# Kernel tuning notes

Measured on AMD Instinct MI355X. Metric: run time of the kernel, lower is better.

## Reference

```python
import jax, jax.numpy as jnp
import numpy as np

D_MODEL = 512
NHEAD = 8
D_HEAD = D_MODEL // NHEAD
SCALE = D_HEAD ** -0.5
EPS = 1e-8


def setup_inputs() -> dict:
    key = jax.random.key(0)
    ks = jax.random.split(key, 12)
    B, N = 4, 2048
    s = D_MODEL ** -0.5
    return {
        "Q_input": jax.random.normal(ks[0], (B, N, D_MODEL), jnp.float32),
        "KV_input": jax.random.normal(ks[1], (B, N, D_MODEL), jnp.float32),
        "SC": jax.random.uniform(ks[2], (B, N, N), jnp.float32),
        "Wq_w": jax.random.normal(ks[3], (D_MODEL, D_MODEL), jnp.float32) * s,
        "Wq_b": jnp.zeros((D_MODEL,), jnp.float32),
        "Wk_w": jax.random.normal(ks[4], (D_MODEL, D_MODEL), jnp.float32) * s,
        "Wk_b": jnp.zeros((D_MODEL,), jnp.float32),
        "Wv_w": jax.random.normal(ks[5], (D_MODEL, D_MODEL), jnp.float32) * s,
        "Wv_b": jnp.zeros((D_MODEL,), jnp.float32),
        "gate_w": jax.random.normal(ks[6], (), jnp.float32),
        "gate_b": jnp.zeros((), jnp.float32),
        "out_w": jax.random.normal(ks[7], (D_MODEL, D_MODEL), jnp.float32) * s,
        "out_b": jnp.zeros((D_MODEL,), jnp.float32),
    }


def reference(Q_input, KV_input, SC, Wq_w, Wq_b, Wk_w, Wk_b, Wv_w, Wv_b,
              gate_w, gate_b, out_w, out_b):
    B, N, _ = Q_input.shape
    # projections -> [B, H, N, d_head]
    def proj(x, w, b):
        y = x @ w.T + b
        return y.reshape(B, N, NHEAD, D_HEAD).transpose(0, 2, 1, 3)
    Q = proj(Q_input, Wq_w, Wq_b)
    K = proj(KV_input, Wk_w, Wk_b)
    V = proj(KV_input, Wv_w, Wv_b)
    # scores [B, H, N, N]
    scores = jnp.einsum('bhqd,bhkd->bhqk', Q, K) * SCALE
    # per-edge gate: sigmoid(w*SC + b), broadcast over heads
    g = jax.nn.sigmoid(SC * gate_w + gate_b)  # [B, N, N]
    scores = scores + jnp.log(g + EPS)[:, None, :, :]
    attn = jax.nn.softmax(scores, axis=-1)
    out = jnp.einsum('bhqk,bhkd->bhqd', attn, V)
    out = out.transpose(0, 2, 1, 3).reshape(B, N, D_MODEL)
    return out @ out_w.T + out_b
```

## Files before the change

kernel.cpp:

```cpp
#include <hip/hip_runtime.h>

typedef unsigned short u16;
typedef unsigned int u32;
typedef __attribute__((ext_vector_type(4))) float f32x4;
typedef __attribute__((ext_vector_type(8))) short s16x8;
typedef __attribute__((ext_vector_type(4))) u16 u16x4;

#define L2E 1.4426950408889634f
#define QSCALE 0.18033688011112042f

__device__ __forceinline__ float bf2f(u16 u) {
    union { u32 i; float f; } v; v.i = ((u32)u) << 16; return v.f;
}
__device__ __forceinline__ u16 f2bf(float f) {
    union { float f; u32 i; } v; v.f = f;
    return (u16)((v.i + 0x7fffu + ((v.i >> 16) & 1u)) >> 16);
}
__device__ __forceinline__ u16 f2bf_rn(float f) {
    union { float f; u32 i; } v; v.f = f;
    return (u16)((v.i + 0x8000u) >> 16);
}

__device__ __forceinline__ void gl2lds16(const u16* g, u16* l) {
    __builtin_amdgcn_global_load_lds(
        (const __attribute__((address_space(1))) void*)g,
        (__attribute__((address_space(3))) void*)l, 16, 0, 0);
}

__global__ __launch_bounds__(256) void conv_kernel(
    const float* __restrict__ s0, const float* __restrict__ s1,
    const float* __restrict__ s2, const float* __restrict__ s3,
    const float* __restrict__ s4, const float* __restrict__ s5,
    u16* __restrict__ dst)
{
    int e = (blockIdx.x * 256 + threadIdx.x) * 4;
    const float* src; int off;
    if      (e < 4194304) { src = s0; off = e; }
    else if (e < 8388608) { src = s1; off = e - 4194304; }
    else if (e < 8650752) { src = s2; off = e - 8388608; }
    else if (e < 8912896) { src = s3; off = e - 8650752; }
    else if (e < 9175040) { src = s4; off = e - 8912896; }
    else                  { src = s5; off = e - 9175040; }
    f32x4 f = *(const f32x4*)(src + off);
    u16x4 o;
#pragma unroll
    for (int j = 0; j < 4; ++j) o[j] = f2bf(f[j]);
    *(u16x4*)(dst + e) = o;
}

__global__ __launch_bounds__(256) void lg_kernel(
    const float* __restrict__ SC, const float* __restrict__ gwp,
    const float* __restrict__ gbp, u16* __restrict__ LGx)
{
    const int flat = blockIdx.x * 256 + threadIdx.x;
    const int lane = flat & 63;
    const int kt   = (flat >> 6) & 31;
    const int t16  = (flat >> 11) & 127;
    const int b    = flat >> 18;
    const int l16 = lane & 15, quad = lane >> 4;
    const float tA = -gwp[0] * L2E, tB = -gbp[0] * L2E;
    const float* row = SC + ((size_t)b * 2048 + t16 * 16 + l16) * 2048
                          + kt * 64 + quad * 4;
    __align__(16) u16 tmp[16];
#pragma unroll
    for (int kk = 0; kk < 4; ++kk) {
        f32x4 x = *(const f32x4*)(row + kk * 16);
#pragma unroll
        for (int reg = 0; reg < 4; ++reg) {
            float g = __builtin_amdgcn_rcpf(
                1.0f + __builtin_amdgcn_exp2f(tA * x[reg] + tB)) + 1e-8f;
            tmp[kk * 4 + reg] = f2bf(__builtin_amdgcn_logf(g));
        }
    }
    u16* dst = LGx + (size_t)flat * 16;
    *(uint4*)dst       = *(uint4*)tmp;
    *(uint4*)(dst + 8) = *(uint4*)(tmp + 8);
}

__device__ __forceinline__ void gemm_core(
    const u16* __restrict__ A, const u16* __restrict__ Bw,
    int m0, int n0, u16* As, u16* Bs, f32x4 acc[4][4])
{
    const int tid = threadIdx.x;
    const int lane = tid & 63, w = tid >> 6;
    const int wm = w >> 1, wn = w & 1;
    const int l16 = lane & 15, quad = lane >> 4;
    const int srow = (lane >> 2), sch = (lane & 3) * 8;
    const f32x4 vzero = {0.f, 0.f, 0.f, 0.f};
#pragma unroll
    for (int i = 0; i < 4; ++i)
#pragma unroll
        for (int j = 0; j < 4; ++j) acc[i][j] = vzero;

    for (int kt = 0; kt < 16; ++kt) {
#pragma unroll
        for (int j = 0; j < 2; ++j) {
            int row = w * 32 + j * 16 + srow;
            gl2lds16(&A[(size_t)(m0 + row) * 512 + kt * 32 + sch],
                     &As[w * 1024 + j * 512]);
            gl2lds16(&Bw[(size_t)(n0 + row) * 512 + kt * 32 + sch],
                     &Bs[w * 1024 + j * 512]);
        }
        __syncthreads();
        s16x8 af[4], bfr[4];
#pragma unroll
        for (int mt = 0; mt < 4; ++mt)
            af[mt] = *(const s16x8*)&As[(wm * 64 + mt * 16 + l16) * 32 + quad * 8];
#pragma unroll
        for (int nt = 0; nt < 4; ++nt)
            bfr[nt] = *(const s16x8*)&Bs[(wn * 64 + nt * 16 + l16) * 32 + quad * 8];
#pragma unroll
        for (int mt = 0; mt < 4; ++mt)
#pragma unroll
            for (int nt = 0; nt < 4; ++nt)
                acc[mt][nt] = __builtin_amdgcn_mfma_f32_16x16x32_bf16(
                    af[mt], bfr[nt], acc[mt][nt], 0, 0, 0);
        __syncthreads();
    }
}

__global__ __launch_bounds__(256) void proj_kernel(
    const u16* __restrict__ cQin, const u16* __restrict__ cKV,
    const u16* __restrict__ cW,
    const float* __restrict__ bq, const float* __restrict__ bk,
    const float* __restrict__ bv,
    u16* __restrict__ Qh, u16* __restrict__ Kh, u16* __restrict__ Vt)
{
    __shared__ __align__(16) u16 As[128 * 32];
    __shared__ __align__(16) u16 Bs[128 * 32];
    const int job = blockIdx.z;
    const u16* A = (job == 0) ? cQin : cKV;
    const u16* W = cW + (size_t)job * 262144;
    const float* bias = (job == 0) ? bq : (job == 1 ? bk : bv);
    const int m0 = blockIdx.y * 128, n0 = blockIdx.x * 128;
    f32x4 acc[4][4];
    gemm_core(A, W, m0, n0, As, Bs, acc);

    const int tid = threadIdx.x, lane = tid & 63, w = tid >> 6;
    const int wm = w >> 1, wn = w & 1, l16 = lane & 15, quad = lane >> 4;
#pragma unroll
    for (int nt = 0; nt < 4; ++nt) {
        int j = n0 + wn * 64 + nt * 16 + l16;
        float bj = bias[j];
        int h = j >> 6, d = j & 63;
#pragma unroll
        for (int mt = 0; mt < 4; ++mt) {
            int trow = m0 + wm * 64 + mt * 16 + quad * 4;
            int bb = trow >> 11, nn = trow & 2047;
            int bh = bb * 8 + h;
            if (job == 2) {
                u16x4 pv;
#pragma unroll
                for (int reg = 0; reg < 4; ++reg) pv[reg] = f2bf(acc[mt][nt][reg] + bj);
                *(u16x4*)&Vt[(size_t)(bh * 64 + d) * 2048 + nn] = pv;
            } else if (job == 0) {
#pragma unroll
                for (int reg = 0; reg < 4; ++reg)
                    Qh[(size_t)(bh * 2048 + nn + reg) * 64 + d] =
                        f2bf((acc[mt][nt][reg] + bj) * QSCALE);
            } else {
#pragma unroll
                for (int reg = 0; reg < 4; ++reg)
                    Kh[(size_t)(bh * 2048 + nn + reg) * 64 + d] =
                        f2bf(acc[mt][nt][reg] + bj);
            }
        }
    }
}

__global__ __launch_bounds__(512, 4) void attn_kernel(
    const u16* __restrict__ Qh, const u16* __restrict__ Kh,
    const u16* __restrict__ Vt, const u16* __restrict__ LGx,
    u16* __restrict__ Ob)
{
    __shared__ __align__(16) u16 Ks[2][4096];
    __shared__ __align__(16) u16 Vs[2][4096];
    __shared__ __align__(16) u16 Plds[8][16][68];
    const int tid = threadIdx.x;
    const int w = tid >> 6, lane = tid & 63;
    const int l16 = lane & 15, quad = lane >> 4;
    const int b = blockIdx.z, head = blockIdx.y, qg = blockIdx.x;
    const int bh = b * 8 + head;
    const int q0 = qg * 128 + w * 16;
    const int t16 = qg * 8 + w;
    const u16* Qp = Qh + (size_t)bh * 131072;
    const u16* Kp = Kh + (size_t)bh * 131072;
    const u16* Vp = Vt + (size_t)bh * 131072;
    const u16* LGt = LGx + ((size_t)((b * 128 + t16) * 32) * 64 + lane) * 16;
    const f32x4 vzero = {0.f, 0.f, 0.f, 0.f};

    const int sr = lane >> 3;
    const int scw = ((lane & 7) ^ sr) * 8;
    const int slab = (w & 3) * 16;
    const bool isK = (w < 4);
    const u16* sG0 = isK ? (Kp + (size_t)(slab + sr) * 64 + scw)
                         : (Vp + (size_t)(slab + sr) * 2048 + scw);
    const u16* sG1 = isK ? (Kp + (size_t)(slab + 8 + sr) * 64 + scw)
                         : (Vp + (size_t)(slab + 8 + sr) * 2048 + scw);
    const size_t sAdv = isK ? 4096 : 64;
    u16* sL0 = isK ? &Ks[0][slab * 64] : &Vs[0][slab * 64];
    u16* sL1 = isK ? &Ks[0][(slab + 8) * 64] : &Vs[0][(slab + 8) * 64];

    s16x8 qf[2];
#pragma unroll
    for (int kc = 0; kc < 2; ++kc)
        qf[kc] = *(const s16x8*)&Qp[(size_t)(q0 + l16) * 64 + kc * 32 + quad * 8];
    f32x4 o[4];
    float lsum = 0.f;
#pragma unroll
    for (int dn = 0; dn < 4; ++dn) o[dn] = vzero;

    gl2lds16(sG0, sL0);
    gl2lds16(sG1, sL1);

    for (int kt = 0; kt < 32; ++kt) {
        __syncthreads();
        const int cur = kt & 1;
        if (kt < 31) {
            const int nxt = cur ^ 1;
            gl2lds16(sG0 + (size_t)(kt + 1) * sAdv, sL0 + nxt * 4096);
            gl2lds16(sG1 + (size_t)(kt + 1) * sAdv, sL1 + nxt * 4096);
        }
        const u16* Kb = &Ks[cur][0];
        const u16* Vb = &Vs[cur][0];
        __align__(16) u16 lgv[16];
        *(uint4*)lgv       = *(const uint4*)(LGt + (size_t)kt * 1024);
        *(uint4*)(lgv + 8) = *(const uint4*)(LGt + (size_t)kt * 1024 + 8);

        f32x4 st[4];
#pragma unroll
        for (int kc = 0; kc < 2; ++kc) {
            s16x8 kf[4];
#pragma unroll
            for (int kk = 0; kk < 4; ++kk)
                kf[kk] = *(const s16x8*)&Kb[(kk * 16 + l16) * 64 +
                                            ((kc * 4 + quad) ^ (l16 & 7)) * 8];
#pragma unroll
            for (int kk = 0; kk < 4; ++kk)
                st[kk] = __builtin_amdgcn_mfma_f32_16x16x32_bf16(
                    kf[kk], qf[kc], kc == 0 ? vzero : st[kk], 0, 0, 0);
        }
#pragma unroll
        for (int kk = 0; kk < 4; ++kk) {
            u16x4 pp;
#pragma unroll
            for (int reg = 0; reg < 4; ++reg) {
                float p = __builtin_amdgcn_exp2f(st[kk][reg] +
                                                 bf2f(lgv[kk * 4 + reg]));
                lsum += p;
                pp[reg] = f2bf_rn(p);
            }
            *(u16x4*)&Plds[w][l16][kk * 16 + quad * 4] = pp;
        }
#pragma unroll
        for (int kc = 0; kc < 2; ++kc) {
            s16x8 pf = *(const s16x8*)&Plds[w][l16][kc * 32 + quad * 8];
            s16x8 vf[4];
#pragma unroll
            for (int dn = 0; dn < 4; ++dn)
                vf[dn] = *(const s16x8*)&Vb[(dn * 16 + l16) * 64 +
                                            ((kc * 4 + quad) ^ (l16 & 7)) * 8];
#pragma unroll
            for (int dn = 0; dn < 4; ++dn)
                o[dn] = __builtin_amdgcn_mfma_f32_16x16x32_bf16(
                    pf, vf[dn], o[dn], 0, 0, 0);
        }
    }
    lsum += __shfl_xor(lsum, 16, 64);
    lsum += __shfl_xor(lsum, 32, 64);
    float inv = __builtin_amdgcn_rcpf(lsum);
#pragma unroll
    for (int reg = 0; reg < 4; ++reg) {
        float invr = __shfl(inv, quad * 4 + reg, 64);
        int trow = b * 2048 + q0 + quad * 4 + reg;
#pragma unroll
        for (int dn = 0; dn < 4; ++dn)
            Ob[(size_t)trow * 512 + head * 64 + dn * 16 + l16] =
                f2bf(o[dn][reg] * invr);
    }
}

__global__ __launch_bounds__(256) void out_kernel(
    const u16* __restrict__ Ob, const u16* __restrict__ cWo,
    const float* __restrict__ bo, float* __restrict__ out)
{
    __shared__ __align__(16) u16 As[128 * 32];
    __shared__ __align__(16) u16 Bs[128 * 32];
    const int m0 = blockIdx.y * 128, n0 = blockIdx.x * 128;
    f32x4 acc[4][4];
    gemm_core(Ob, cWo, m0, n0, As, Bs, acc);
    const int tid = threadIdx.x, lane = tid & 63, w = tid >> 6;
    const int wm = w >> 1, wn = w & 1, l16 = lane & 15, quad = lane >> 4;
#pragma unroll
    for (int nt = 0; nt < 4; ++nt) {
        int j = n0 + wn * 64 + nt * 16 + l16;
        float bj = bo[j];
#pragma unroll
        for (int mt = 0; mt < 4; ++mt) {
            int t = m0 + wm * 64 + mt * 16 + quad * 4;
#pragma unroll
            for (int reg = 0; reg < 4; ++reg)
                out[(size_t)(t + reg) * 512 + j] = acc[mt][nt][reg] + bj;
        }
    }
}

extern "C" void kernel_launch(void* const* d_in, const int* in_sizes, int n_in,
                              void* d_out, int out_size, void* d_ws, size_t ws_size,
                              hipStream_t stream)
{
    const float* Qin  = (const float*)d_in[0];
    const float* KVin = (const float*)d_in[1];
    const float* SC   = (const float*)d_in[2];
    const float* Wq   = (const float*)d_in[3];
    const float* bq   = (const float*)d_in[4];
    const float* Wk   = (const float*)d_in[5];
    const float* bk   = (const float*)d_in[6];
    const float* Wv   = (const float*)d_in[7];
    const float* bv   = (const float*)d_in[8];
    const float* gw   = (const float*)d_in[9];
    const float* gb   = (const float*)d_in[10];
    const float* Wo   = (const float*)d_in[11];
    const float* bo   = (const float*)d_in[12];
    float* out = (float*)d_out;

    u16* conv = (u16*)d_ws;
    u16* cQin = conv;
    u16* cKV  = conv + 4194304;
    u16* cW   = conv + 8388608;
    u16* Qh   = conv + 9437184;
    u16* Kh   = Qh + 4194304;
    u16* Vt   = Kh + 4194304;
    u16* Ob   = Vt + 4194304;
    u16* LGx  = Ob + 4194304;

    hipLaunchKernelGGL(conv_kernel, dim3(9216), dim3(256), 0, stream,
                       Qin, KVin, Wq, Wk, Wv, Wo, conv);
    hipLaunchKernelGGL(lg_kernel, dim3(4096), dim3(256), 0, stream,
                       SC, gw, gb, LGx);
    hipLaunchKernelGGL(proj_kernel, dim3(4, 64, 3), dim3(256), 0, stream,
                       cQin, cKV, cW, bq, bk, bv, Qh, Kh, Vt);
    hipLaunchKernelGGL(attn_kernel, dim3(16, 8, 4), dim3(512), 0, stream,
                       Qh, Kh, Vt, LGx, Ob);
    hipLaunchKernelGGL(out_kernel, dim3(4, 64), dim3(256), 0, stream,
                       Ob, cW + 786432, bo, out);
}
```

Before: 261.9 us.

## Merge prep kernels, double-buffer GEMM LDS, MFMA row sums, truncating bf16 pack

The conversion and log-gate kernels are merged into one launch, which removes a kernel boundary. The shared GEMM core now double-buffers its LDS tiles so the next K slice loads while the current one computes, and it drops one barrier per iteration. In attention, the softmax row sum is computed with an MFMA against a ones vector instead of scalar adds and shuffles, and P is packed to bf16 by truncation. The cost is more LDS per GEMM block, a slightly different rounding of P, and an extra MFMA per chunk.

```diff
diff --git a/kernel.cpp b/kernel.cpp
--- a/kernel.cpp
+++ b/kernel.cpp
@@ -16,9 +16,9 @@
     union { float f; u32 i; } v; v.f = f;
     return (u16)((v.i + 0x7fffu + ((v.i >> 16) & 1u)) >> 16);
 }
-__device__ __forceinline__ u16 f2bf_rn(float f) {
-    union { float f; u32 i; } v; v.f = f;
-    return (u16)((v.i + 0x8000u) >> 16);
+__device__ __forceinline__ u32 pack_hi(float a, float b) {
+    union { float f; u32 i; } x, y; x.f = a; y.f = b;
+    return (x.i >> 16) | (y.i & 0xFFFF0000u);
 }
 
 __device__ __forceinline__ void gl2lds16(const u16* g, u16* l) {
@@ -27,54 +27,53 @@
         (__attribute__((address_space(3))) void*)l, 16, 0, 0);
 }
 
-__global__ __launch_bounds__(256) void conv_kernel(
+__global__ __launch_bounds__(256) void prep_kernel(
     const float* __restrict__ s0, const float* __restrict__ s1,
     const float* __restrict__ s2, const float* __restrict__ s3,
     const float* __restrict__ s4, const float* __restrict__ s5,
-    u16* __restrict__ dst)
-{
-    int e = (blockIdx.x * 256 + threadIdx.x) * 4;
-    const float* src; int off;
-    if      (e < 4194304) { src = s0; off = e; }
-    else if (e < 8388608) { src = s1; off = e - 4194304; }
-    else if (e < 8650752) { src = s2; off = e - 8388608; }
-    else if (e < 8912896) { src = s3; off = e - 8650752; }
-    else if (e < 9175040) { src = s4; off = e - 8912896; }
-    else                  { src = s5; off = e - 9175040; }
-    f32x4 f = *(const f32x4*)(src + off);
-    u16x4 o;
-#pragma unroll
-    for (int j = 0; j < 4; ++j) o[j] = f2bf(f[j]);
-    *(u16x4*)(dst + e) = o;
-}
-
-__global__ __launch_bounds__(256) void lg_kernel(
+    u16* __restrict__ dst,
     const float* __restrict__ SC, const float* __restrict__ gwp,
     const float* __restrict__ gbp, u16* __restrict__ LGx)
 {
-    const int flat = blockIdx.x * 256 + threadIdx.x;
-    const int lane = flat & 63;
-    const int kt   = (flat >> 6) & 31;
-    const int t16  = (flat >> 11) & 127;
-    const int b    = flat >> 18;
-    const int l16 = lane & 15, quad = lane >> 4;
-    const float tA = -gwp[0] * L2E, tB = -gbp[0] * L2E;
-    const float* row = SC + ((size_t)b * 2048 + t16 * 16 + l16) * 2048
-                          + kt * 64 + quad * 4;
-    __align__(16) u16 tmp[16];
-#pragma unroll
-    for (int kk = 0; kk < 4; ++kk) {
-        f32x4 x = *(const f32x4*)(row + kk * 16);
-#pragma unroll
-        for (int reg = 0; reg < 4; ++reg) {
-            float g = __builtin_amdgcn_rcpf(
-                1.0f + __builtin_amdgcn_exp2f(tA * x[reg] + tB)) + 1e-8f;
-            tmp[kk * 4 + reg] = f2bf(__builtin_amdgcn_logf(g));
-        }
-    }
-    u16* dst = LGx + (size_t)flat * 16;
-    *(uint4*)dst       = *(uint4*)tmp;
-    *(uint4*)(dst + 8) = *(uint4*)(tmp + 8);
+    if (blockIdx.x < 9216) {
+        int e = (blockIdx.x * 256 + threadIdx.x) * 4;
+        const float* src; int off;
+        if      (e < 4194304) { src = s0; off = e; }
+        else if (e < 8388608) { src = s1; off = e - 4194304; }
+        else if (e < 8650752) { src = s2; off = e - 8388608; }
+        else if (e < 8912896) { src = s3; off = e - 8650752; }
+        else if (e < 9175040) { src = s4; off = e - 8912896; }
+        else                  { src = s5; off = e - 9175040; }
+        f32x4 f = *(const f32x4*)(src + off);
+        u16x4 o;
+#pragma unroll
+        for (int j = 0; j < 4; ++j) o[j] = f2bf(f[j]);
+        *(u16x4*)(dst + e) = o;
+    } else {
+        const int flat = (blockIdx.x - 9216) * 256 + threadIdx.x;
+        const int lane = flat & 63;
+        const int kt   = (flat >> 6) & 31;
+        const int t16  = (flat >> 11) & 127;
+        const int b    = flat >> 18;
+        const int l16 = lane & 15, quad = lane >> 4;
+        const float tA = -gwp[0] * L2E, tB = -gbp[0] * L2E;
+        const float* row = SC + ((size_t)b * 2048 + t16 * 16 + l16) * 2048
+                              + kt * 64 + quad * 4;
+        __align__(16) u16 tmp[16];
+#pragma unroll
+        for (int kk = 0; kk < 4; ++kk) {
+            f32x4 x = *(const f32x4*)(row + kk * 16);
+#pragma unroll
+            for (int reg = 0; reg < 4; ++reg) {
+                float g = __builtin_amdgcn_rcpf(
+                    1.0f + __builtin_amdgcn_exp2f(tA * x[reg] + tB)) + 1e-8f;
+                tmp[kk * 4 + reg] = f2bf(__builtin_amdgcn_logf(g));
+            }
+        }
+        u16* d = LGx + (size_t)flat * 16;
+        *(uint4*)d       = *(uint4*)tmp;
+        *(uint4*)(d + 8) = *(uint4*)(tmp + 8);
+    }
 }
 
 __device__ __forceinline__ void gemm_core(
@@ -92,30 +91,39 @@
 #pragma unroll
         for (int j = 0; j < 4; ++j) acc[i][j] = vzero;
 
+#pragma unroll
+    for (int j = 0; j < 2; ++j) {
+        int row = w * 32 + j * 16 + srow;
+        gl2lds16(&A[(size_t)(m0 + row) * 512 + sch], &As[w * 1024 + j * 512]);
+        gl2lds16(&Bw[(size_t)(n0 + row) * 512 + sch], &Bs[w * 1024 + j * 512]);
+    }
     for (int kt = 0; kt < 16; ++kt) {
-#pragma unroll
-        for (int j = 0; j < 2; ++j) {
-            int row = w * 32 + j * 16 + srow;
-            gl2lds16(&A[(size_t)(m0 + row) * 512 + kt * 32 + sch],
-                     &As[w * 1024 + j * 512]);
-            gl2lds16(&Bw[(size_t)(n0 + row) * 512 + kt * 32 + sch],
-                     &Bs[w * 1024 + j * 512]);
-        }
         __syncthreads();
+        const int cur = (kt & 1) * 4096;
+        if (kt < 15) {
+            const int nxt = ((kt + 1) & 1) * 4096;
+#pragma unroll
+            for (int j = 0; j < 2; ++j) {
+                int row = w * 32 + j * 16 + srow;
+                gl2lds16(&A[(size_t)(m0 + row) * 512 + (kt + 1) * 32 + sch],
+                         &As[nxt + w * 1024 + j * 512]);
+                gl2lds16(&Bw[(size_t)(n0 + row) * 512 + (kt + 1) * 32 + sch],
+                         &Bs[nxt + w * 1024 + j * 512]);
+            }
+        }
         s16x8 af[4], bfr[4];
 #pragma unroll
         for (int mt = 0; mt < 4; ++mt)
-            af[mt] = *(const s16x8*)&As[(wm * 64 + mt * 16 + l16) * 32 + quad * 8];
+            af[mt] = *(const s16x8*)&As[cur + (wm * 64 + mt * 16 + l16) * 32 + quad * 8];
 #pragma unroll
         for (int nt = 0; nt < 4; ++nt)
-            bfr[nt] = *(const s16x8*)&Bs[(wn * 64 + nt * 16 + l16) * 32 + quad * 8];
+            bfr[nt] = *(const s16x8*)&Bs[cur + (wn * 64 + nt * 16 + l16) * 32 + quad * 8];
 #pragma unroll
         for (int mt = 0; mt < 4; ++mt)
 #pragma unroll
             for (int nt = 0; nt < 4; ++nt)
                 acc[mt][nt] = __builtin_amdgcn_mfma_f32_16x16x32_bf16(
                     af[mt], bfr[nt], acc[mt][nt], 0, 0, 0);
-        __syncthreads();
     }
 }
 
@@ -126,8 +134,8 @@
     const float* __restrict__ bv,
     u16* __restrict__ Qh, u16* __restrict__ Kh, u16* __restrict__ Vt)
 {
-    __shared__ __align__(16) u16 As[128 * 32];
-    __shared__ __align__(16) u16 Bs[128 * 32];
+    __shared__ __align__(16) u16 As[2 * 4096];
+    __shared__ __align__(16) u16 Bs[2 * 4096];
     const int job = blockIdx.z;
     const u16* A = (job == 0) ? cQin : cKV;
     const u16* W = cW + (size_t)job * 262144;
@@ -188,6 +196,8 @@
     const u16* Vp = Vt + (size_t)bh * 131072;
     const u16* LGt = LGx + ((size_t)((b * 128 + t16) * 32) * 64 + lane) * 16;
     const f32x4 vzero = {0.f, 0.f, 0.f, 0.f};
+    const s16x8 ones = {0x3F80, 0x3F80, 0x3F80, 0x3F80,
+                        0x3F80, 0x3F80, 0x3F80, 0x3F80};
 
     const int sr = lane >> 3;
     const int scw = ((lane & 7) ^ sr) * 8;
@@ -205,8 +215,7 @@
 #pragma unroll
     for (int kc = 0; kc < 2; ++kc)
         qf[kc] = *(const s16x8*)&Qp[(size_t)(q0 + l16) * 64 + kc * 32 + quad * 8];
-    f32x4 o[4];
-    float lsum = 0.f;
+    f32x4 o[4], lacc = vzero;
 #pragma unroll
     for (int dn = 0; dn < 4; ++dn) o[dn] = vzero;
 
@@ -242,19 +251,17 @@
         }
 #pragma unroll
         for (int kk = 0; kk < 4; ++kk) {
-            u16x4 pp;
-#pragma unroll
-            for (int reg = 0; reg < 4; ++reg) {
-                float p = __builtin_amdgcn_exp2f(st[kk][reg] +
-                                                 bf2f(lgv[kk * 4 + reg]));
-                lsum += p;
-                pp[reg] = f2bf_rn(p);
-            }
-            *(u16x4*)&Plds[w][l16][kk * 16 + quad * 4] = pp;
+            float p0 = __builtin_amdgcn_exp2f(st[kk][0] + bf2f(lgv[kk * 4 + 0]));
+            float p1 = __builtin_amdgcn_exp2f(st[kk][1] + bf2f(lgv[kk * 4 + 1]));
+            float p2 = __builtin_amdgcn_exp2f(st[kk][2] + bf2f(lgv[kk * 4 + 2]));
+            float p3 = __builtin_amdgcn_exp2f(st[kk][3] + bf2f(lgv[kk * 4 + 3]));
+            uint2 pk = {pack_hi(p0, p1), pack_hi(p2, p3)};
+            *(uint2*)&Plds[w][l16][kk * 16 + quad * 4] = pk;
         }
 #pragma unroll
         for (int kc = 0; kc < 2; ++kc) {
             s16x8 pf = *(const s16x8*)&Plds[w][l16][kc * 32 + quad * 8];
+            lacc = __builtin_amdgcn_mfma_f32_16x16x32_bf16(pf, ones, lacc, 0, 0, 0);
             s16x8 vf[4];
 #pragma unroll
             for (int dn = 0; dn < 4; ++dn)
@@ -266,17 +273,14 @@
                     pf, vf[dn], o[dn], 0, 0, 0);
         }
     }
-    lsum += __shfl_xor(lsum, 16, 64);
-    lsum += __shfl_xor(lsum, 32, 64);
-    float inv = __builtin_amdgcn_rcpf(lsum);
 #pragma unroll
     for (int reg = 0; reg < 4; ++reg) {
-        float invr = __shfl(inv, quad * 4 + reg, 64);
+        float inv = __builtin_amdgcn_rcpf(lacc[reg]);
         int trow = b * 2048 + q0 + quad * 4 + reg;
 #pragma unroll
         for (int dn = 0; dn < 4; ++dn)
             Ob[(size_t)trow * 512 + head * 64 + dn * 16 + l16] =
-                f2bf(o[dn][reg] * invr);
+                f2bf(o[dn][reg] * inv);
     }
 }
 
@@ -284,8 +288,8 @@
     const u16* __restrict__ Ob, const u16* __restrict__ cWo,
     const float* __restrict__ bo, float* __restrict__ out)
 {
-    __shared__ __align__(16) u16 As[128 * 32];
-    __shared__ __align__(16) u16 Bs[128 * 32];
+    __shared__ __align__(16) u16 As[2 * 4096];
+    __shared__ __align__(16) u16 Bs[2 * 4096];
     const int m0 = blockIdx.y * 128, n0 = blockIdx.x * 128;
     f32x4 acc[4][4];
     gemm_core(Ob, cWo, m0, n0, As, Bs, acc);
@@ -334,10 +338,8 @@
     u16* Ob   = Vt + 4194304;
     u16* LGx  = Ob + 4194304;
 
-    hipLaunchKernelGGL(conv_kernel, dim3(9216), dim3(256), 0, stream,
-                       Qin, KVin, Wq, Wk, Wv, Wo, conv);
-    hipLaunchKernelGGL(lg_kernel, dim3(4096), dim3(256), 0, stream,
-                       SC, gw, gb, LGx);
+    hipLaunchKernelGGL(prep_kernel, dim3(13312), dim3(256), 0, stream,
+                       Qin, KVin, Wq, Wk, Wv, Wo, conv, SC, gw, gb, LGx);
     hipLaunchKernelGGL(proj_kernel, dim3(4, 64, 3), dim3(256), 0, stream,
                        cQin, cKV, cW, bq, bk, bv, Qh, Kh, Vt);
     hipLaunchKernelGGL(attn_kernel, dim3(16, 8, 4), dim3(512), 0, stream,
```

After: 244.1 us. 6.8% less time.
